# Performance work log

Hardware: AMD Instinct MI355X
Metric: run time of the kernel (lower is better)

The kernel has to match this reference:

```python
import jax, jax.numpy as jnp
import numpy as np
from jax import lax

LBDA = 0.1
EPS = 0.01
NUM_CLASSES = 20


def setup_inputs() -> dict:
    key = jax.random.key(0)
    k1, k2 = jax.random.split(key)
    target_features = jax.random.normal(k1, (2048, 8, 2048), dtype=jnp.float32)
    support_features = jax.random.normal(k2, (100, 8, 2048), dtype=jnp.float32)
    # 20-way 5-shot: every class present so per-class mean is well defined
    support_labels = jnp.repeat(jnp.arange(NUM_CLASSES, dtype=jnp.int32), 100 // NUM_CLASSES)
    return {
        "target_features": target_features,
        "support_features": support_features,
        "support_labels": support_labels,
    }


def _softmin(xs, lbda):
    # -lbda * log(sum_i exp(-x_i/lbda)), stable
    return -lbda * jax.nn.logsumexp(jnp.stack([-x / lbda for x in xs], axis=0), axis=0)


def otam_cum_dist(dists, lbda=LBDA):
    # dists: [Q, Sp, L, S] frame distance matrices
    d = jnp.pad(dists, ((0, 0), (0, 0), (0, 0), (1, 1)))  # pad columns -> M = S + 2
    M = d.shape[-1]
    # row 0: running sum along columns (cum[0,0] = d[0,0] = 0 from padding)
    row0 = jnp.cumsum(d[:, :, 0, :], axis=-1)

    def step(prev_row, d_row):
        # prev_row, d_row: [Q, Sp, M]; column 0 is never written -> stays 0
        cur = [jnp.zeros_like(d_row[..., 0])]
        cur.append(d_row[..., 1] + _softmin([prev_row[..., 0], prev_row[..., 1], cur[0]], lbda))
        for m in range(2, M - 1):
            cur.append(d_row[..., m] + _softmin([prev_row[..., m - 1], cur[m - 1]], lbda))
        cur.append(d_row[..., M - 1] + _softmin([prev_row[..., M - 2], prev_row[..., M - 1], cur[M - 2]], lbda))
        new_row = jnp.stack(cur, axis=-1)
        return new_row, None

    d_rows = jnp.moveaxis(d[:, :, 1:, :], 2, 0)  # [L-1, Q, Sp, M]
    final_row, _ = lax.scan(step, row0, d_rows)
    return final_row[..., -1]  # [Q, Sp]


def cos_sim(x, y, eps=EPS):
    num = x @ y.T
    den = jnp.linalg.norm(x, axis=-1)[:, None] * jnp.linalg.norm(y, axis=-1)[None, :] + eps
    return num / den


def reference(target_features, support_features, support_labels):
    Q, S, D = target_features.shape
    Sp = support_features.shape[0]
    tf = target_features.reshape(Q * S, D)
    sf = support_features.reshape(Sp * S, D)
    frame_dists = 1.0 - cos_sim(tf, sf)  # [Q*S, Sp*S]
    # '(tb ts) (sb ss) -> tb sb ts ss'
    dists = frame_dists.reshape(Q, S, Sp, S).transpose(0, 2, 1, 3)
    cum_dists = otam_cum_dist(dists) + otam_cum_dist(dists.transpose(0, 1, 3, 2))  # [Q, Sp]
    # per-class mean over support (torch.unique returns sorted labels 0..C-1)
    onehot = (support_labels[:, None] == jnp.arange(NUM_CLASSES)[None, :]).astype(cum_dists.dtype)
    onehot = onehot / jnp.sum(onehot, axis=0, keepdims=True)
    class_dists = cum_dists @ onehot  # [Q, C]
    return -class_dists[None]  # logits [1, Q, C]
```

## Files before the change

### kernel.cpp

```cpp
#include <hip/hip_runtime.h>

#define QN    2048
#define SS    8
#define DD    2048
#define SP    100
#define NCLS  20
#define MROWS (QN*SS)
#define NROWS (SP*SS)
#define NPAD  896
#define KK    DD

typedef __bf16 bf16x8 __attribute__((ext_vector_type(8)));
typedef float  f32x4  __attribute__((ext_vector_type(4)));

__device__ __forceinline__ unsigned short f2bf(float f) {
    unsigned int u = __float_as_uint(f);
    u += 0x7fffu + ((u >> 16) & 1u);
    return (unsigned short)(u >> 16);
}

__global__ void cvt_kernel(const float* __restrict__ tf, const float* __restrict__ sf,
                           unsigned short* __restrict__ Abf, unsigned short* __restrict__ Bbf,
                           float* __restrict__ nA, float* __restrict__ nB)
{
    int row = blockIdx.x;
    int tid = threadIdx.x;
    const float* src = nullptr;
    unsigned short* dst;
    float* nrm; int r;
    if (row < MROWS) { src = tf + (size_t)row * DD; dst = Abf + (size_t)row * DD; nrm = nA; r = row; }
    else {
        r = row - MROWS;
        dst = Bbf + (size_t)r * DD; nrm = nB;
        if (r < NROWS) src = sf + (size_t)r * DD;
    }
    float s = 0.f;
    union { uint4 u; unsigned short h[8]; } pk;
    if (src) {
        float4 v0 = *(const float4*)(src + tid * 8);
        float4 v1 = *(const float4*)(src + tid * 8 + 4);
        s = v0.x*v0.x + v0.y*v0.y + v0.z*v0.z + v0.w*v0.w
          + v1.x*v1.x + v1.y*v1.y + v1.z*v1.z + v1.w*v1.w;
        pk.h[0]=f2bf(v0.x); pk.h[1]=f2bf(v0.y); pk.h[2]=f2bf(v0.z); pk.h[3]=f2bf(v0.w);
        pk.h[4]=f2bf(v1.x); pk.h[5]=f2bf(v1.y); pk.h[6]=f2bf(v1.z); pk.h[7]=f2bf(v1.w);
    } else {
        pk.u = make_uint4(0, 0, 0, 0);
    }
    *(uint4*)(dst + (size_t)tid * 8) = pk.u;

    for (int o = 32; o; o >>= 1) s += __shfl_down(s, o);
    __shared__ float red[4];
    if ((tid & 63) == 0) red[tid >> 6] = s;
    __syncthreads();
    if (tid == 0) nrm[r] = sqrtf(red[0] + red[1] + red[2] + red[3]);
}

__device__ __forceinline__ float softmin2(float a, float b) {
    float mn = fminf(a, b), mx = fmaxf(a, b);
    return mn - 0.1f * __logf(1.0f + __expf((mn - mx) * 10.0f));
}
__device__ __forceinline__ float softmin3(float a, float b, float c) {
    float mn = fminf(fminf(a, b), c);
    float sum = __expf((mn - a) * 10.0f) + __expf((mn - b) * 10.0f) + __expf((mn - c) * 10.0f);
    return mn - 0.1f * __logf(sum);
}

__device__ __forceinline__ void gld16(const void* g, void* l) {
    __builtin_amdgcn_global_load_lds(
        (const __attribute__((address_space(1))) unsigned int*)g,
        (__attribute__((address_space(3))) unsigned int*)l, 16, 0, 0);
}

#define EPB (32 * 65)

__global__ __launch_bounds__(256, 2) void gemm_kernel(
    const unsigned short* __restrict__ A,
    const unsigned short* __restrict__ B,
    const float* __restrict__ nA, const float* __restrict__ nB,
    float* __restrict__ cum)
{
    __shared__ __align__(16) char smem[4 * EPB * 4];
    unsigned short* Als = (unsigned short*)smem;
    unsigned short* Bls = Als + 128 * 32;

    const int mt  = blockIdx.x;
    const int nt  = blockIdx.y;
    const int tid = threadIdx.x;
    const int lane = tid & 63;
    const int w    = tid >> 6;
    const int wm   = (w & 1) * 64, wn = (w >> 1) * 64;
    const int col  = lane & 15, kg = lane >> 4;

    f32x4 acc[4][4] = {};

    const int c0 = tid, c1 = tid + 256;
    const int r0 = c0 >> 2, k0 = ((c0 & 3) ^ ((c0 >> 3) & 3)) * 8;
    const int r1 = c1 >> 2, k1 = ((c1 & 3) ^ ((c1 >> 3) & 3)) * 8;
    const unsigned short* Ab0 = A + (size_t)mt * 128 * KK + (size_t)r0 * KK + k0;
    const unsigned short* Ab1 = A + (size_t)mt * 128 * KK + (size_t)r1 * KK + k1;
    const unsigned short* Bb0 = B + (size_t)nt * 128 * KK + (size_t)r0 * KK + k0;
    const unsigned short* Bb1 = B + (size_t)nt * 128 * KK + (size_t)r1 * KK + k1;

    const int ksw = (kg ^ ((col >> 1) & 3)) * 8;

    for (int kk = 0; kk < KK; kk += 32) {
        __syncthreads();
        gld16(Ab0 + kk, (char*)Als + c0 * 16);
        gld16(Ab1 + kk, (char*)Als + c1 * 16);
        gld16(Bb0 + kk, (char*)Bls + c0 * 16);
        gld16(Bb1 + kk, (char*)Bls + c1 * 16);
        __syncthreads();
        bf16x8 af[4], bfr[4];
#pragma unroll
        for (int i = 0; i < 4; i++) af[i]  = *(const bf16x8*)(Als + (wm + i * 16 + col) * 32 + ksw);
#pragma unroll
        for (int i = 0; i < 4; i++) bfr[i] = *(const bf16x8*)(Bls + (wn + i * 16 + col) * 32 + ksw);
#pragma unroll
        for (int mi = 0; mi < 4; mi++)
#pragma unroll
            for (int ni = 0; ni < 4; ni++)
                acc[mi][ni] = __builtin_amdgcn_mfma_f32_16x16x32_bf16(af[mi], bfr[ni], acc[mi][ni], 0, 0, 0);
    }

    const int mbase = mt * 128 + wm;
    const int nbase = nt * 128 + wn;
    const int qv0 = mt * 16 + (wm >> 3);
    const int sv0 = nt * 16 + (wn >> 3);
    float* eb = (float*)smem + w * EPB;

    const int qv2 = (lane >> 3) & 3;
    const int sv  = lane & 7;
    const int dir = lane >> 5;

#pragma unroll
    for (int p = 0; p < 2; p++) {
        __syncthreads();
#pragma unroll
        for (int mi2 = 0; mi2 < 2; mi2++) {
            const int mi = p * 2 + mi2;
            const float nx0 = nA[mbase + mi * 16 + kg * 4 + 0];
            const float nx1 = nA[mbase + mi * 16 + kg * 4 + 1];
            const float nx2 = nA[mbase + mi * 16 + kg * 4 + 2];
            const float nx3 = nA[mbase + mi * 16 + kg * 4 + 3];
#pragma unroll
            for (int ni = 0; ni < 4; ni++) {
                const float ny = nB[nbase + ni * 16 + col];
                float* dstp = eb + (mi2 * 16 + kg * 4) * 65 + ni * 16 + col;
                dstp[0]      = 1.0f - acc[mi][ni][0] / (nx0 * ny + 0.01f);
                dstp[65]     = 1.0f - acc[mi][ni][1] / (nx1 * ny + 0.01f);
                dstp[130]    = 1.0f - acc[mi][ni][2] / (nx2 * ny + 0.01f);
                dstp[195]    = 1.0f - acc[mi][ni][3] / (nx3 * ny + 0.01f);
            }
        }
        __syncthreads();

        const float* tb = eb + (qv2 * 8) * 65 + sv * 8;
        float prev[10], cur[10];
        prev[0] = 0.f;
#pragma unroll
        for (int m = 1; m <= 8; m++)
            prev[m] = prev[m - 1] + (dir ? tb[(m - 1) * 65] : tb[m - 1]);
        prev[9] = prev[8];
#pragma unroll
        for (int l = 1; l < 8; l++) {
            float d[8];
#pragma unroll
            for (int j = 0; j < 8; j++) d[j] = dir ? tb[j * 65 + l] : tb[l * 65 + j];
            cur[0] = 0.f;
            cur[1] = d[0] + softmin3(prev[0], prev[1], 0.0f);
#pragma unroll
            for (int m = 2; m <= 8; m++)
                cur[m] = d[m - 1] + softmin2(prev[m - 1], cur[m - 1]);
            cur[9] = softmin3(prev[8], prev[9], cur[8]);
#pragma unroll
            for (int m = 0; m < 10; m++) prev[m] = cur[m];
        }
        float res = prev[9];
        res += __shfl_down(res, 32);
        if (dir == 0) {
            const int qg = qv0 + p * 4 + qv2;
            const int sg = sv0 + sv;
            if (sg < SP) cum[(size_t)qg * SP + sg] = res;
        }
    }
}

__global__ void cls_kernel(const float* __restrict__ cum, const int* __restrict__ labels,
                           float* __restrict__ out)
{
    int idx = blockIdx.x * 256 + threadIdx.x;
    int q = idx / NCLS, c = idx % NCLS;
    float s = 0.f; int n = 0;
    const float* row = cum + (size_t)q * SP;
    for (int sp = 0; sp < SP; sp++) {
        if (labels[sp] == c) { s += row[sp]; n++; }
    }
    out[idx] = -s / (float)n;
}

extern "C" void kernel_launch(void* const* d_in, const int* in_sizes, int n_in,
                              void* d_out, int out_size, void* d_ws, size_t ws_size,
                              hipStream_t stream)
{
    const float* tf     = (const float*)d_in[0];
    const float* sf     = (const float*)d_in[1];
    const int*   labels = (const int*)d_in[2];
    float* out = (float*)d_out;

    char* ws = (char*)d_ws;
    const size_t szA    = (size_t)MROWS * KK * 2;
    const size_t szB    = (size_t)NPAD  * KK * 2;
    const size_t szNA   = (size_t)MROWS * 4;
    const size_t szNB   = (size_t)NPAD  * 4;
    unsigned short* Abf = (unsigned short*)ws;
    unsigned short* Bbf = (unsigned short*)(ws + szA);
    float* nA   = (float*)(ws + szA + szB);
    float* nB   = (float*)(ws + szA + szB + szNA);
    float* cum  = (float*)(ws + szA + szB + szNA + szNB);

    cvt_kernel<<<MROWS + NPAD, 256, 0, stream>>>(tf, sf, Abf, Bbf, nA, nB);
    gemm_kernel<<<dim3(128, 7), 256, 0, stream>>>(Abf, Bbf, nA, nB, cum);
    cls_kernel<<<160, 256, 0, stream>>>(cum, labels, out);
}
```

Before: 319.1 us.

## Shrink GEMM M-tile to 64, store distance tiles as bf16, raise occupancy

Halves the M tile of the fused GEMM plus OTAM kernel from 128 to 64 rows, so each wave keeps 2x4 accumulators and the launch bound allows 4 blocks per CU. The grid doubles to 256x7 blocks. The epilogue now writes frame distances to LDS as bf16 with a 72-element stride in a single pass, and each lane loads its 8x8 tile into registers once as raw vectors before the DP. The XOR swizzle on LDS loads is also dropped. The aim is more occupancy and less LDS and register pressure, at the cost of losing precision in the distances fed to the DP, possible LDS bank conflicts, and lower operand reuse per block.

Result: no change. 322.2 us (+1.0%).

```diff
diff --git a/kernel.cpp b/kernel.cpp
--- a/kernel.cpp
+++ b/kernel.cpp
@@ -9,6 +9,8 @@
 #define NROWS (SP*SS)
 #define NPAD  896
 #define KK    DD
+#define MT    64
+#define NT    128
 
 typedef __bf16 bf16x8 __attribute__((ext_vector_type(8)));
 typedef float  f32x4  __attribute__((ext_vector_type(4)));
@@ -71,117 +73,118 @@
         (__attribute__((address_space(3))) unsigned int*)l, 16, 0, 0);
 }
 
-#define EPB (32 * 65)
-
-__global__ __launch_bounds__(256, 2) void gemm_kernel(
+__device__ __forceinline__ float cellf(const uint4* raw, int a, int b) {
+    const unsigned* p = (const unsigned*)raw;
+    unsigned wv = p[a * 4 + (b >> 1)];
+    return __uint_as_float((b & 1) ? (wv & 0xffff0000u) : (wv << 16));
+}
+
+#define EBS (32 * 72)
+
+__global__ __launch_bounds__(256, 4) void gemm_kernel(
     const unsigned short* __restrict__ A,
     const unsigned short* __restrict__ B,
     const float* __restrict__ nA, const float* __restrict__ nB,
     float* __restrict__ cum)
 {
-    __shared__ __align__(16) char smem[4 * EPB * 4];
-    unsigned short* Als = (unsigned short*)smem;
-    unsigned short* Bls = Als + 128 * 32;
+    __shared__ __align__(16) unsigned short smem[4 * EBS];
+    unsigned short* Als = smem;
+    unsigned short* Bls = smem + MT * 32;
 
     const int mt  = blockIdx.x;
     const int nt  = blockIdx.y;
     const int tid = threadIdx.x;
     const int lane = tid & 63;
     const int w    = tid >> 6;
-    const int wm   = (w & 1) * 64, wn = (w >> 1) * 64;
+    const int wm   = (w & 1) * 32, wn = (w >> 1) * 64;
     const int col  = lane & 15, kg = lane >> 4;
 
-    f32x4 acc[4][4] = {};
-
-    const int c0 = tid, c1 = tid + 256;
-    const int r0 = c0 >> 2, k0 = ((c0 & 3) ^ ((c0 >> 3) & 3)) * 8;
-    const int r1 = c1 >> 2, k1 = ((c1 & 3) ^ ((c1 >> 3) & 3)) * 8;
-    const unsigned short* Ab0 = A + (size_t)mt * 128 * KK + (size_t)r0 * KK + k0;
-    const unsigned short* Ab1 = A + (size_t)mt * 128 * KK + (size_t)r1 * KK + k1;
-    const unsigned short* Bb0 = B + (size_t)nt * 128 * KK + (size_t)r0 * KK + k0;
-    const unsigned short* Bb1 = B + (size_t)nt * 128 * KK + (size_t)r1 * KK + k1;
-
-    const int ksw = (kg ^ ((col >> 1) & 3)) * 8;
+    f32x4 acc[2][4] = {};
+
+    const int rr = tid >> 2, ks = (tid & 3) * 8;
+    const unsigned short* Ap  = A + (size_t)(mt * MT  + rr) * KK + ks;
+    const unsigned short* Bp0 = B + (size_t)(nt * NT  + rr) * KK + ks;
+    const unsigned short* Bp1 = B + (size_t)(nt * NT + 64 + rr) * KK + ks;
 
     for (int kk = 0; kk < KK; kk += 32) {
         __syncthreads();
-        gld16(Ab0 + kk, (char*)Als + c0 * 16);
-        gld16(Ab1 + kk, (char*)Als + c1 * 16);
-        gld16(Bb0 + kk, (char*)Bls + c0 * 16);
-        gld16(Bb1 + kk, (char*)Bls + c1 * 16);
+        gld16(Ap  + kk, (char*)Als + tid * 16);
+        gld16(Bp0 + kk, (char*)Bls + tid * 16);
+        gld16(Bp1 + kk, (char*)Bls + (tid + 256) * 16);
         __syncthreads();
-        bf16x8 af[4], bfr[4];
-#pragma unroll
-        for (int i = 0; i < 4; i++) af[i]  = *(const bf16x8*)(Als + (wm + i * 16 + col) * 32 + ksw);
-#pragma unroll
-        for (int i = 0; i < 4; i++) bfr[i] = *(const bf16x8*)(Bls + (wn + i * 16 + col) * 32 + ksw);
-#pragma unroll
-        for (int mi = 0; mi < 4; mi++)
+        bf16x8 af[2], bfr[4];
+#pragma unroll
+        for (int i = 0; i < 2; i++) af[i]  = *(const bf16x8*)(Als + (wm + i * 16 + col) * 32 + kg * 8);
+#pragma unroll
+        for (int i = 0; i < 4; i++) bfr[i] = *(const bf16x8*)(Bls + (wn + i * 16 + col) * 32 + kg * 8);
+#pragma unroll
+        for (int mi = 0; mi < 2; mi++)
 #pragma unroll
             for (int ni = 0; ni < 4; ni++)
                 acc[mi][ni] = __builtin_amdgcn_mfma_f32_16x16x32_bf16(af[mi], bfr[ni], acc[mi][ni], 0, 0, 0);
     }
 
-    const int mbase = mt * 128 + wm;
-    const int nbase = nt * 128 + wn;
-    const int qv0 = mt * 16 + (wm >> 3);
-    const int sv0 = nt * 16 + (wn >> 3);
-    float* eb = (float*)smem + w * EPB;
-
-    const int qv2 = (lane >> 3) & 3;
-    const int sv  = lane & 7;
-    const int dir = lane >> 5;
-
-#pragma unroll
-    for (int p = 0; p < 2; p++) {
-        __syncthreads();
-#pragma unroll
-        for (int mi2 = 0; mi2 < 2; mi2++) {
-            const int mi = p * 2 + mi2;
-            const float nx0 = nA[mbase + mi * 16 + kg * 4 + 0];
-            const float nx1 = nA[mbase + mi * 16 + kg * 4 + 1];
-            const float nx2 = nA[mbase + mi * 16 + kg * 4 + 2];
-            const float nx3 = nA[mbase + mi * 16 + kg * 4 + 3];
-#pragma unroll
-            for (int ni = 0; ni < 4; ni++) {
-                const float ny = nB[nbase + ni * 16 + col];
-                float* dstp = eb + (mi2 * 16 + kg * 4) * 65 + ni * 16 + col;
-                dstp[0]      = 1.0f - acc[mi][ni][0] / (nx0 * ny + 0.01f);
-                dstp[65]     = 1.0f - acc[mi][ni][1] / (nx1 * ny + 0.01f);
-                dstp[130]    = 1.0f - acc[mi][ni][2] / (nx2 * ny + 0.01f);
-                dstp[195]    = 1.0f - acc[mi][ni][3] / (nx3 * ny + 0.01f);
+    __syncthreads();
+
+    unsigned short* eb = smem + w * EBS;
+    const int mbase = mt * MT + wm;
+    const int nbase = nt * NT + wn;
+
+#pragma unroll
+    for (int mi = 0; mi < 2; mi++) {
+        float nx[4];
+#pragma unroll
+        for (int r = 0; r < 4; r++) nx[r] = nA[mbase + mi * 16 + kg * 4 + r];
+#pragma unroll
+        for (int ni = 0; ni < 4; ni++) {
+            const float ny = nB[nbase + ni * 16 + col];
+#pragma unroll
+            for (int r = 0; r < 4; r++) {
+                float d = 1.0f - acc[mi][ni][r] / (nx[r] * ny + 0.01f);
+                eb[(mi * 16 + kg * 4 + r) * 72 + ni * 16 + col] = f2bf(d);
             }
         }
-        __syncthreads();
-
-        const float* tb = eb + (qv2 * 8) * 65 + sv * 8;
-        float prev[10], cur[10];
-        prev[0] = 0.f;
-#pragma unroll
-        for (int m = 1; m <= 8; m++)
-            prev[m] = prev[m - 1] + (dir ? tb[(m - 1) * 65] : tb[m - 1]);
-        prev[9] = prev[8];
-#pragma unroll
-        for (int l = 1; l < 8; l++) {
-            float d[8];
-#pragma unroll
-            for (int j = 0; j < 8; j++) d[j] = dir ? tb[j * 65 + l] : tb[l * 65 + j];
-            cur[0] = 0.f;
-            cur[1] = d[0] + softmin3(prev[0], prev[1], 0.0f);
-#pragma unroll
-            for (int m = 2; m <= 8; m++)
-                cur[m] = d[m - 1] + softmin2(prev[m - 1], cur[m - 1]);
-            cur[9] = softmin3(prev[8], prev[9], cur[8]);
-#pragma unroll
-            for (int m = 0; m < 10; m++) prev[m] = cur[m];
+    }
+
+    const int pr  = lane & 31;
+    const int qv2 = pr >> 3, sv = pr & 7;
+    const int dir = lane >> 5;
+
+    uint4 raw[8];
+    const unsigned short* tb = eb + (qv2 * 8) * 72 + sv * 8;
+#pragma unroll
+    for (int l = 0; l < 8; l++) raw[l] = *(const uint4*)(tb + l * 72);
+
+    float prev[10], cur[10];
+    prev[0] = 0.f;
+#pragma unroll
+    for (int m = 1; m <= 8; m++) {
+        float v0 = cellf(raw, 0, m - 1), v1 = cellf(raw, m - 1, 0);
+        prev[m] = prev[m - 1] + (dir ? v1 : v0);
+    }
+    prev[9] = prev[8];
+#pragma unroll
+    for (int l = 1; l < 8; l++) {
+        float d[8];
+#pragma unroll
+        for (int j = 0; j < 8; j++) {
+            float v0 = cellf(raw, l, j), v1 = cellf(raw, j, l);
+            d[j] = dir ? v1 : v0;
         }
-        float res = prev[9];
-        res += __shfl_down(res, 32);
-        if (dir == 0) {
-            const int qg = qv0 + p * 4 + qv2;
-            const int sg = sv0 + sv;
-            if (sg < SP) cum[(size_t)qg * SP + sg] = res;
-        }
+        cur[1] = d[0] + softmin3(prev[0], prev[1], 0.0f);
+#pragma unroll
+        for (int m = 2; m <= 8; m++)
+            cur[m] = d[m - 1] + softmin2(prev[m - 1], cur[m - 1]);
+        cur[9] = softmin3(prev[8], prev[9], cur[8]);
+#pragma unroll
+        for (int m = 1; m < 10; m++) prev[m] = cur[m];
+    }
+    float res = prev[9];
+    res += __shfl_down(res, 32);
+    if (dir == 0) {
+        const int qg = mt * 8 + (wm >> 3) + qv2;
+        const int sg = nt * 16 + (wn >> 3) + sv;
+        if (sg < SP) cum[(size_t)qg * SP + sg] = res;
     }
 }
 
@@ -219,6 +222,6 @@
     float* cum  = (float*)(ws + szA + szB + szNA + szNB);
 
     cvt_kernel<<<MROWS + NPAD, 256, 0, stream>>>(tf, sf, Abf, Bbf, nA, nB);
-    gemm_kernel<<<dim3(128, 7), 256, 0, stream>>>(Abf, Bbf, nA, nB, cum);
+    gemm_kernel<<<dim3(MROWS / MT, NPAD / NT), 256, 0, stream>>>(Abf, Bbf, nA, nB, cum);
     cls_kernel<<<160, 256, 0, stream>>>(cum, labels, out);
 }
```
